# Kernel optimization log

Measured on AMD Instinct MI355X. Metric: run time of the kernel, lower is better.

Reference implementation:

```python
import jax, jax.numpy as jnp
import numpy as np
from math import factorial as fact

L, P, T, CIN, COUT, N = 4, 5, 15, 32, 32, 1000


def _cg(j1, m1, j2, m2, J, M):
    # Clebsch-Gordan coefficient <j1 m1 j2 m2 | J M> (integer args, Racah formula)
    if m1 + m2 != M or not (abs(j1 - j2) <= J <= j1 + j2):
        return 0.0
    if abs(m1) > j1 or abs(m2) > j2 or abs(M) > J:
        return 0.0
    pre = (2.0 * J + 1.0) * fact(J + j1 - j2) * fact(J - j1 + j2) * fact(j1 + j2 - J) / fact(j1 + j2 + J + 1)
    pre *= fact(J + M) * fact(J - M) * fact(j1 - m1) * fact(j1 + m1) * fact(j2 - m2) * fact(j2 + m2)
    s = 0.0
    for k in range(0, j1 + j2 - J + 1):
        d = (k, j1 + j2 - J - k, j1 - m1 - k, j2 + m2 - k, J - j2 + m1 + k, J - j1 - m2 + k)
        if min(d) < 0:
            continue
        den = 1.0
        for x in d:
            den *= fact(x)
        s += (-1.0) ** k / den
    return float(np.sqrt(pre) * s)


def _precompute(Ldeg):
    # Mirrors PrecomputingTensorsForConv6D
    tensors, coefs = [], []
    for l in range(Ldeg):
        for l1 in range(Ldeg):
            for l2 in range(abs(l - l1), min(Ldeg, l + l1 + 1)):
                coefs.append(8.0 * np.pi ** 2 / (2 * l1 + 1)
                             * np.sqrt((2 * l + 1) * (2 * l1 + 1) / (4.0 * np.pi * (2 * l2 + 1)))
                             * _cg(l, 0, l1, 0, l2, 0))
                T1 = np.zeros((l + 1, l1 + 1, l2 + 1)); T2 = np.zeros_like(T1); T3 = np.zeros_like(T1)
                for k in range(l + 1):
                    for k1 in range(l1 + 1):
                        if abs(k + k1) < l2 + 1:
                            T1[k, k1, k + k1] = _cg(l, k, l1, k1, l2, k + k1) * (-1) ** k1
                        if k1 > 0 and abs(k - k1) < l2 + 1:
                            if k - k1 >= 0:
                                T2[k, k1, k - k1] = _cg(l, k, l1, -k1, l2, k - k1) * (-1) ** l1
                            else:
                                T3[k, k1, k1 - k] = (-1) ** (k1 - k) * (-1) ** (l1 + l2) * _cg(l, k, l1, -k1, l2, k - k1)
                tensors.append((jnp.asarray(T1, jnp.float32), jnp.asarray(T2, jnp.float32), jnp.asarray(T3, jnp.float32)))
    return tensors, np.asarray(coefs, np.float64)

_TENSORS, _COEFS = _precompute(L)


def setup_inputs() -> dict:
    key = jax.random.key(0)
    ks = iter(jax.random.split(key, 64))
    inp = {}
    for l in range(L):
        inp[f"in{l}_real"] = 0.1 * jax.random.normal(next(ks), (N, T, l + 1, P, CIN), jnp.float32)
        inp[f"in{l}_imag"] = 0.1 * jax.random.normal(next(ks), (N, T, l + 1, P, CIN), jnp.float32)
    for l in range(L):
        inp[f"w{l}_real"] = 0.05 * jax.random.normal(next(ks), (l + 1, T, P, CIN, COUT), jnp.float32)
        inp[f"w{l}_imag"] = 0.05 * jax.random.normal(next(ks), (l + 1, T, P, CIN, COUT), jnp.float32)
    for l in range(L):
        inp[f"b{l}_real"] = jax.random.uniform(next(ks), (1, l + 1, P, COUT), jnp.float32, -0.05, 0.05)
        inp[f"b{l}_imag"] = jax.random.uniform(next(ks), (1, l + 1, P, COUT), jnp.float32, -0.05, 0.05)
    return inp


def _forward(ins, ws_raw, bs_raw):
    # Mask imaginary parts: weight order-0 row (k=0) and bias degree-0 component are zeroed,
    # exactly as the temp_term masks in build().
    ws, bs = [], []
    for l in range(L):
        wmask = jnp.ones((l + 1, 1, 1, 1, 1), jnp.float32).at[0].set(0.0)
        ws += [ws_raw[2 * l], ws_raw[2 * l + 1] * wmask]
        bmask = jnp.ones((1, l + 1, 1, 1), jnp.float32).at[:, 0].set(0.0)
        bs += [bs_raw[2 * l], bs_raw[2 * l + 1] * bmask]
    outputs = []
    itr = 0
    for l in range(L):
        out_r = 0.0
        out_i = 0.0
        for l1 in range(L):
            for l2 in range(abs(l - l1), min(L, l + l1 + 1)):
                c = float(_COEFS[itr])
                T1, T2, T3 = _TENSORS[itr]
                xr, xi = ins[2 * l2], ins[2 * l2 + 1]      # [N, T, l2+1, P, Cin]
                wr, wi = ws[2 * l1], ws[2 * l1 + 1]        # [l1+1, T, P, Cin, Cout]
                # complex CG contraction -> [N, l+1, P, Cout]
                out_r = out_r + c * jnp.einsum('lmk,ntkpi,mtpij->nlpj', T1 + T2 + T3, xr, wr)
                out_r = out_r - c * jnp.einsum('lmk,ntkpi,mtpij->nlpj', T1 - T2 + T3, xi, wi)
                out_i = out_i + c * jnp.einsum('lmk,ntkpi,mtpij->nlpj', T1 - T2 - T3, xr, wi)
                out_i = out_i + c * jnp.einsum('lmk,ntkpi,mtpij->nlpj', T1 + T2 - T3, xi, wr)
                itr += 1
        outputs.append(out_r + bs[2 * l])
        outputs.append(out_i + bs[2 * l + 1])
    return tuple(outputs)


def reference(in0_real, in0_imag, in1_real, in1_imag, in2_real, in2_imag, in3_real, in3_imag,
              w0_real, w0_imag, w1_real, w1_imag, w2_real, w2_imag, w3_real, w3_imag,
              b0_real, b0_imag, b1_real, b1_imag, b2_real, b2_imag, b3_real, b3_imag):
    ins = [in0_real, in0_imag, in1_real, in1_imag, in2_real, in2_imag, in3_real, in3_imag]
    ws = [w0_real, w0_imag, w1_real, w1_imag, w2_real, w2_imag, w3_real, w3_imag]
    bs = [b0_real, b0_imag, b1_real, b1_imag, b2_real, b2_imag, b3_real, b3_imag]
    return _forward(ins, ws, bs)
```

## Files before the change

### kernel.cpp

```cpp
#include <hip/hip_runtime.h>
#include <hip/hip_bf16.h>

#define NB   1000
#define NPAD 1024
#define TT   15
#define PP   5
#define CI   32
#define CO   32
#define KDIM 9600
#define MDIM 640
#define NCHUNK 300
#define NCOL   20
#define TABN  16384
#define KSTEPS 150
#define WTELEMS 1536000
#define XCVT_BLOCKS 24000
#define WTR_BLOCKS (WTELEMS / 256)
#define TAB_BLOCKS (TABN / 256)

typedef __attribute__((ext_vector_type(8))) short          bf16x8;
typedef __attribute__((ext_vector_type(8))) unsigned short ushort8;
typedef __attribute__((ext_vector_type(4))) float          f32x4;

struct Chunks {
  short ci[NCHUNK]; short l2[NCHUNK]; short t[NCHUNK]; short k2[NCHUNK];
  short xidx[NCHUNK]; short cls[NCHUNK]; int ns[NCHUNK]; int offc[NCHUNK];
};
constexpr Chunks mkchunks() {
  Chunks c{};
  int idx = 0;
  for (int l2 = 0; l2 < 4; ++l2)
    for (int ci = 0; ci < 2; ++ci)
      for (int t = 0; t < TT; ++t)
        for (int k2 = 0; k2 <= l2; ++k2) {
          c.ci[idx] = (short)ci; c.l2[idx] = (short)l2;
          c.t[idx] = (short)t;   c.k2[idx] = (short)k2;
          c.xidx[idx] = (short)(2 * l2 + ci);
          c.cls[idx]  = (short)(l2 * (l2 + 1) / 2 + k2);
          c.ns[idx]   = TT * (l2 + 1) * PP * CI;
          c.offc[idx] = (t * (l2 + 1) + k2) * PP * CI;
          ++idx;
        }
  return c;
}
__constant__ Chunks g_ck = mkchunks();

struct Cols { int l[NCOL]; int lm[NCOL]; int ci[NCOL]; long obase[NCOL]; };
constexpr Cols mkcols() {
  Cols c{};
  long acc = 0; int idx = 0;
  for (int l = 0; l < 4; ++l)
    for (int ci = 0; ci < 2; ++ci) {
      for (int lm = 0; lm <= l; ++lm) {
        c.l[idx] = l; c.lm[idx] = lm; c.ci[idx] = ci; c.obase[idx] = acc; ++idx;
      }
      acc += (long)NB * (l + 1) * PP * CO;
    }
  return c;
}
__constant__ Cols g_cols = mkcols();

constexpr int wtsize(int tensor) { return ((tensor >> 1) + 1) * TT * PP * CI * CO; }
struct WOffs { int off[8]; int sz[8]; };
constexpr WOffs mkwoffs() {
  WOffs w{}; int acc = 0;
  for (int i = 0; i < 8; ++i) { w.off[i] = acc; w.sz[i] = wtsize(i); acc += w.sz[i]; }
  return w;
}
__constant__ WOffs g_wo = mkwoffs();

__constant__ short g_l1of[10] = {0,1,1,2,2,2,3,3,3,3};
__constant__ short g_mof[10]  = {0,0,1,0,1,2,0,1,2,3};

__device__ double dfact(int n) { double r = 1.0; for (int i = 2; i <= n; ++i) r *= i; return r; }

__device__ double dcg(int j1, int m1, int j2, int m2, int J, int M) {
  if (m1 + m2 != M) return 0.0;
  int lo = j1 - j2; if (lo < 0) lo = -lo;
  if (J < lo || J > j1 + j2) return 0.0;
  int am1 = m1 < 0 ? -m1 : m1, am2 = m2 < 0 ? -m2 : m2, aM = M < 0 ? -M : M;
  if (am1 > j1 || am2 > j2 || aM > J) return 0.0;
  double pre = (2.0 * J + 1.0) * dfact(J + j1 - j2) * dfact(J - j1 + j2) * dfact(j1 + j2 - J)
               / dfact(j1 + j2 + J + 1);
  pre *= dfact(J + M) * dfact(J - M) * dfact(j1 - m1) * dfact(j1 + m1) * dfact(j2 - m2) * dfact(j2 + m2);
  double s = 0.0;
  for (int k = 0; k <= j1 + j2 - J; ++k) {
    int d1 = j1 + j2 - J - k, d2 = j1 - m1 - k, d3 = j2 + m2 - k,
        d4 = J - j2 + m1 + k, d5 = J - j1 - m2 + k;
    if (d1 < 0 || d2 < 0 || d3 < 0 || d4 < 0 || d5 < 0) continue;
    double den = dfact(k) * dfact(d1) * dfact(d2) * dfact(d3) * dfact(d4) * dfact(d5);
    s += ((k & 1) ? -1.0 : 1.0) / den;
  }
  return sqrt(pre) * s;
}

struct PArgs { const float* w[8]; const float* x[8]; float* wt; float* tab; unsigned short* xb; };

__global__ __launch_bounds__(256) void k_prep(PArgs A) {
  const int bx = blockIdx.x, tid = threadIdx.x;
  if (bx < XCVT_BLOCKS) {
    int slot = bx * 256 + tid;
    int i8 = slot % 1200;
    int rest = slot / 1200;
    int n = rest & (NPAD - 1);
    int p = rest >> 10;
    int kk = i8 * 8;
    ushort8 o;
    if (n < NB) {
      int chunk = kk >> 5;
      const float* xp = A.x[g_ck.xidx[chunk]] + (size_t)n * g_ck.ns[chunk]
                        + g_ck.offc[chunk] + p * CI + (kk & 31);
      float4 v0 = *(const float4*)xp;
      float4 v1 = *(const float4*)(xp + 4);
      float f[8] = {v0.x, v0.y, v0.z, v0.w, v1.x, v1.y, v1.z, v1.w};
      #pragma unroll
      for (int e = 0; e < 8; ++e) {
        unsigned u = __float_as_uint(f[e]);
        u += 0x7fff + ((u >> 16) & 1);
        o[e] = (unsigned short)(u >> 16);
      }
    } else {
      #pragma unroll
      for (int e = 0; e < 8; ++e) o[e] = 0;
    }
    *(ushort8*)(A.xb + ((size_t)(p * NPAD + n)) * KDIM + kk) = o;
  } else if (bx < XCVT_BLOCKS + WTR_BLOCKS) {
    int e = (bx - XCVT_BLOCKS) * 256 + tid;
    int tensor = 0;
    #pragma unroll
    for (int q = 1; q < 8; ++q) if (e >= g_wo.off[q]) tensor = q;
    int le = e - g_wo.off[tensor];
    int i = le & 31;
    int t = (le >> 5) % TT;
    int r = le / (32 * TT);
    int j = r & 31;
    int p = (r >> 5) % PP;
    int m = r / (32 * PP);
    A.wt[e] = A.w[tensor][(((m * TT + t) * PP + p) * CI + i) * CO + j];
  } else {
    int idx = (bx - XCVT_BLOCKS - WTR_BLOCKS) * 256 + tid;
    int k2 = idx & 3, m = (idx >> 2) & 3, lm = (idx >> 4) & 3, l2 = (idx >> 6) & 3,
        l1 = (idx >> 8) & 3, l = (idx >> 10) & 3, combo = (idx >> 12) & 3;
    float v = 0.f;
    int dlo = l - l1; if (dlo < 0) dlo = -dlo;
    bool valid = (lm <= l) && (m <= l1) && (k2 <= l2) && (l2 >= dlo) && (l2 <= l + l1);
    if (valid) {
      const double PI = 3.14159265358979323846;
      double coef = 8.0 * PI * PI / (2.0 * l1 + 1.0)
                    * sqrt((2.0 * l + 1.0) * (2.0 * l1 + 1.0) / (4.0 * PI * (2.0 * l2 + 1.0)))
                    * dcg(l, 0, l1, 0, l2, 0);
      double t1 = 0.0, t2 = 0.0, t3 = 0.0;
      if (k2 == lm + m)
        t1 = dcg(l, lm, l1, m, l2, k2) * ((m & 1) ? -1.0 : 1.0);
      if (m > 0 && lm - m >= 0 && k2 == lm - m)
        t2 = dcg(l, lm, l1, -m, l2, lm - m) * ((l1 & 1) ? -1.0 : 1.0);
      if (m > 0 && lm - m < 0 && k2 == m - lm)
        t3 = (((m - lm) & 1) ? -1.0 : 1.0) * (((l1 + l2) & 1) ? -1.0 : 1.0)
             * dcg(l, lm, l1, -m, l2, lm - m);
      double r = 0.0;
      if (combo == 0) r =  coef * (t1 + t2 + t3);
      else if (combo == 1) r = -coef * (t1 - t2 + t3);
      else if (combo == 2) r =  coef * (t1 - t2 - t3);
      else r = coef * (t1 + t2 - t3);
      v = (float)r;
    }
    A.tab[idx] = v;
  }
}

struct FArgs { const float* wt; const float* tab; unsigned short* weffT; };

__global__ __launch_bounds__(256) void k_fold(FArgs A) {
  const int tid = threadIdx.x;
  const int mo = blockIdx.x, p = blockIdx.y;
  const int j = mo & 31, col = mo >> 5;
  const int l = g_cols.l[col], lm = g_cols.lm[col], cio = g_cols.ci[col];
  __shared__ float ldsW[2][10][480];
  __shared__ float ldsC[2][10][10];

  for (int e = tid; e < 2 * 10 * 480; e += 256) {
    int ti = e % 480;
    int rowid = e / 480;
    int wci = rowid / 10, r = rowid % 10;
    int l1 = g_l1of[r], m = g_mof[r];
    ldsW[wci][r][ti] = A.wt[g_wo.off[2 * l1 + wci] + m * (PP * CO * TT * CI)
                            + (p * CO + j) * (TT * CI) + ti];
  }
  if (tid < 200) {
    int r = tid % 10, clk = (tid / 10) % 10, ci = tid / 100;
    int l1 = g_l1of[r], m = g_mof[r];
    int l2 = g_l1of[clk], k2 = g_mof[clk];
    int combo = cio * 2 + ci, wci = cio ^ ci;
    float v = 0.f;
    int dlo = l - l1; if (dlo < 0) dlo = -dlo;
    if (l2 >= dlo && l2 <= l + l1 && m <= l1 && k2 <= l2)
      v = A.tab[(((((combo * 4 + l) * 4 + l1) * 4 + l2) * 4 + lm) * 4 + m) * 4 + k2];
    if (wci == 1 && m == 0) v = 0.f;
    ldsC[ci][clk][r] = v;
  }
  __syncthreads();

  unsigned short* dst = A.weffT + ((size_t)(p * MDIM + mo)) * KDIM;
  for (int kk = tid; kk < KDIM; kk += 256) {
    int chunk = kk >> 5, i = kk & 31;
    int ci = g_ck.ci[chunk], t = g_ck.t[chunk], cls = g_ck.cls[chunk];
    int wci = cio ^ ci;
    float s = 0.f;
    #pragma unroll
    for (int r = 0; r < 10; ++r)
      s += ldsC[ci][cls][r] * ldsW[wci][r][t * 32 + i];
    unsigned u = __float_as_uint(s);
    u += 0x7fff + ((u >> 16) & 1);
    dst[kk] = (unsigned short)(u >> 16);
  }
}

__device__ __forceinline__ void gl_lds16(const void* g, void* l) {
  __builtin_amdgcn_global_load_lds(
      (const __attribute__((address_space(1))) unsigned int*)g,
      (__attribute__((address_space(3))) unsigned int*)l, 16, 0, 0);
}

struct GArgs { const unsigned short* xb; const unsigned short* weffT; float* partial; int nsplit; };

__global__ __launch_bounds__(256, 4) void k_gemm(GArgs A) {
  const int tid = threadIdx.x;
  const int lane = tid & 63;
  const int wv = tid >> 6, wr = wv >> 1, wc = wv & 1;
  const int n0 = blockIdx.x * 128, mo0 = blockIdx.y * 128;
  const int zz = blockIdx.z;
  const int NS = A.nsplit;
  const int p = zz / NS, sp = zz % NS;
  const int bsteps = KSTEPS / NS, rem = KSTEPS % NS;
  const int mysteps = bsteps + (sp < rem ? 1 : 0);
  const int sstart = sp * bsteps + (sp < rem ? sp : rem);

  __shared__ __align__(16) unsigned short sA[128 * 64];
  __shared__ __align__(16) unsigned short sB[128 * 64];
  f32x4 acc[4][4] = {};

  int aoff[4];
  #pragma unroll
  for (int u = 0; u < 4; ++u) {
    int s = u * 256 + tid;
    int row = s >> 3;
    int qs = (s & 7) ^ (row & 7);
    aoff[u] = row * KDIM + qs * 8;
  }
  const unsigned short* xbase = A.xb + (size_t)p * NPAD * KDIM + (size_t)n0 * KDIM + sstart * 64;
  const unsigned short* wbase = A.weffT + (size_t)p * MDIM * KDIM + (size_t)mo0 * KDIM + sstart * 64;

  for (int cc = 0; cc < mysteps; ++cc) {
    const unsigned short* xs = xbase + cc * 64;
    const unsigned short* ws = wbase + cc * 64;
    #pragma unroll
    for (int u = 0; u < 4; ++u) {
      gl_lds16(xs + aoff[u], (void*)(sA + (u * 256 + tid) * 8));
      gl_lds16(ws + aoff[u], (void*)(sB + (u * 256 + tid) * 8));
    }
    __syncthreads();
    #pragma unroll
    for (int ks = 0; ks < 2; ++ks) {
      const int q = ks * 4 + (lane >> 4);
      bf16x8 af[4], bfr[4];
      #pragma unroll
      for (int m = 0; m < 4; ++m) {
        int ra = wr * 64 + m * 16 + (lane & 15);
        af[m] = *(const bf16x8*)(sA + ra * 64 + ((q ^ (ra & 7)) << 3));
      }
      #pragma unroll
      for (int n = 0; n < 4; ++n) {
        int rb = wc * 64 + n * 16 + (lane & 15);
        bfr[n] = *(const bf16x8*)(sB + rb * 64 + ((q ^ (rb & 7)) << 3));
      }
      #pragma unroll
      for (int m = 0; m < 4; ++m)
        #pragma unroll
        for (int n = 0; n < 4; ++n)
          acc[m][n] = __builtin_amdgcn_mfma_f32_16x16x32_bf16(af[m], bfr[n], acc[m][n], 0, 0, 0);
    }
    __syncthreads();
  }

  float* pout = A.partial + (size_t)zz * (NPAD * MDIM);
  #pragma unroll
  for (int m = 0; m < 4; ++m) {
    #pragma unroll
    for (int nn = 0; nn < 4; ++nn) {
      int mo = mo0 + wc * 64 + nn * 16 + (lane & 15);
      #pragma unroll
      for (int r = 0; r < 4; ++r) {
        int n = n0 + wr * 64 + m * 16 + (lane >> 4) * 4 + r;
        pout[(size_t)n * MDIM + mo] = acc[m][nn][r];
      }
    }
  }
}

struct RArgs { const float* partial; const float* b[8]; float* out; int nsplit; };

__global__ __launch_bounds__(256) void k_red(RArgs A) {
  int e4 = blockIdx.x * 256 + threadIdx.x;
  if (e4 >= NB * (MDIM / 4) * PP) return;
  int mo4 = e4 % (MDIM / 4);
  int rest = e4 / (MDIM / 4);
  int n = rest % NB;
  int p = rest / NB;
  int mo = mo4 * 4;
  float4 s = make_float4(0.f, 0.f, 0.f, 0.f);
  for (int sp = 0; sp < A.nsplit; ++sp) {
    float4 v = *(const float4*)&A.partial[((size_t)(p * A.nsplit + sp) * NPAD + n) * MDIM + mo];
    s.x += v.x; s.y += v.y; s.z += v.z; s.w += v.w;
  }
  int colid = mo >> 5, j = mo & 31;
  int l = g_cols.l[colid], lmv = g_cols.lm[colid], cio = g_cols.ci[colid];
  long base = g_cols.obase[colid];
  float4 bias = *(const float4*)&A.b[2 * l + cio][(lmv * PP + p) * CO + j];
  if (cio == 1 && lmv == 0) bias = make_float4(0.f, 0.f, 0.f, 0.f);
  float4 o = make_float4(s.x + bias.x, s.y + bias.y, s.z + bias.z, s.w + bias.w);
  *(float4*)&A.out[base + (((size_t)n * (l + 1) + lmv) * PP + p) * CO + j] = o;
}

extern "C" void kernel_launch(void* const* d_in, const int* in_sizes, int n_in,
                              void* d_out, int out_size, void* d_ws, size_t ws_size,
                              hipStream_t stream) {
  float* tab = (float*)d_ws;
  float* wt  = tab + TABN;
  unsigned short* weffT = (unsigned short*)(wt + WTELEMS);
  unsigned short* xb    = weffT + (size_t)PP * MDIM * KDIM;
  float* partial = (float*)(xb + (size_t)PP * NPAD * KDIM);

  size_t base_bytes = (size_t)TABN * 4 + (size_t)WTELEMS * 4
                    + (size_t)PP * MDIM * KDIM * 2 + (size_t)PP * NPAD * KDIM * 2;
  size_t per_split = (size_t)PP * NPAD * MDIM * 4;
  int NS = 1;
  for (int c = 5; c >= 2; --c)
    if (ws_size >= base_bytes + (size_t)c * per_split) { NS = c; break; }

  PArgs pa;
  for (int i = 0; i < 8; ++i) pa.w[i] = (const float*)d_in[8 + i];
  for (int i = 0; i < 8; ++i) pa.x[i] = (const float*)d_in[i];
  pa.wt = wt; pa.tab = tab; pa.xb = xb;
  k_prep<<<dim3(XCVT_BLOCKS + WTR_BLOCKS + TAB_BLOCKS), dim3(256), 0, stream>>>(pa);

  FArgs fa;
  fa.wt = wt; fa.tab = (const float*)tab; fa.weffT = weffT;
  k_fold<<<dim3(MDIM, PP), dim3(256), 0, stream>>>(fa);

  GArgs ga;
  ga.xb = xb; ga.weffT = weffT; ga.partial = partial; ga.nsplit = NS;
  k_gemm<<<dim3(8, 5, 5 * NS), dim3(256), 0, stream>>>(ga);

  RArgs ra;
  ra.partial = partial; ra.out = (float*)d_out; ra.nsplit = NS;
  for (int i = 0; i < 8; ++i) ra.b[i] = (const float*)d_in[16 + i];
  k_red<<<dim3((NB * (MDIM / 4) * PP + 255) / 256), dim3(256), 0, stream>>>(ra);
}
```

Measured before the change: 267.1 us.

## Widen x conversion per thread, LDS-tile weight transpose, remap GEMM blocks per XCD

The x-to-bf16 conversion now has each thread handle a full 32-channel chunk with eight float4 loads and four 16-byte stores, which cuts the block count. The weight transpose now goes through a shared-memory tile, so both global reads and writes are coalesced instead of scattered gathers. The GEMM launch is flattened to 1D and block indices are remapped so consecutive blocks on the same XCD (blockIdx mod 8) share the same z-slice, which should improve L2 reuse. The catch is added index arithmetic and a shared-memory allocation in k_prep that every branch of the kernel pays for, not just the transpose branch.

```diff
diff --git a/kernel.cpp b/kernel.cpp
--- a/kernel.cpp
+++ b/kernel.cpp
@@ -14,8 +14,8 @@
 #define TABN  16384
 #define KSTEPS 150
 #define WTELEMS 1536000
-#define XCVT_BLOCKS 24000
-#define WTR_BLOCKS (WTELEMS / 256)
+#define XCVT_BLOCKS 6000
+#define WTRX_BLOCKS 300
 #define TAB_BLOCKS (TABN / 256)
 
 typedef __attribute__((ext_vector_type(8))) short          bf16x8;
@@ -71,6 +71,8 @@
 
 __constant__ short g_l1of[10] = {0,1,1,2,2,2,3,3,3,3};
 __constant__ short g_mof[10]  = {0,0,1,0,1,2,0,1,2,3};
+__constant__ short g_wtT[20] = {0,1,2,2,3,3,4,4,4,5,5,5,6,6,6,6,7,7,7,7};
+__constant__ short g_wtM[20] = {0,0,0,1,0,1,0,1,2,0,1,2,0,1,2,3,0,1,2,3};
 
 __device__ double dfact(int n) { double r = 1.0; for (int i = 2; i <= n; ++i) r *= i; return r; }
 
@@ -98,47 +100,65 @@
 
 __global__ __launch_bounds__(256) void k_prep(PArgs A) {
   const int bx = blockIdx.x, tid = threadIdx.x;
+  __shared__ float lds[5][32][33];
+
   if (bx < XCVT_BLOCKS) {
-    int slot = bx * 256 + tid;
-    int i8 = slot % 1200;
-    int rest = slot / 1200;
+    int g = bx * 256 + tid;
+    int chunk = g % 300;
+    int rest = g / 300;
     int n = rest & (NPAD - 1);
     int p = rest >> 10;
-    int kk = i8 * 8;
-    ushort8 o;
+    ushort8* dst = (ushort8*)(A.xb + ((size_t)(p * NPAD + n)) * KDIM + chunk * 32);
     if (n < NB) {
-      int chunk = kk >> 5;
       const float* xp = A.x[g_ck.xidx[chunk]] + (size_t)n * g_ck.ns[chunk]
-                        + g_ck.offc[chunk] + p * CI + (kk & 31);
-      float4 v0 = *(const float4*)xp;
-      float4 v1 = *(const float4*)(xp + 4);
-      float f[8] = {v0.x, v0.y, v0.z, v0.w, v1.x, v1.y, v1.z, v1.w};
-      #pragma unroll
-      for (int e = 0; e < 8; ++e) {
-        unsigned u = __float_as_uint(f[e]);
-        u += 0x7fff + ((u >> 16) & 1);
-        o[e] = (unsigned short)(u >> 16);
+                        + g_ck.offc[chunk] + p * CI;
+      float4 v[8];
+      #pragma unroll
+      for (int e = 0; e < 8; ++e) v[e] = *(const float4*)(xp + 4 * e);
+      #pragma unroll
+      for (int q = 0; q < 4; ++q) {
+        float4 a = v[2 * q], b = v[2 * q + 1];
+        float fa[8] = {a.x, a.y, a.z, a.w, b.x, b.y, b.z, b.w};
+        ushort8 o;
+        #pragma unroll
+        for (int e = 0; e < 8; ++e) {
+          unsigned u = __float_as_uint(fa[e]);
+          u += 0x7fff + ((u >> 16) & 1);
+          o[e] = (unsigned short)(u >> 16);
+        }
+        dst[q] = o;
       }
     } else {
-      #pragma unroll
-      for (int e = 0; e < 8; ++e) o[e] = 0;
-    }
-    *(ushort8*)(A.xb + ((size_t)(p * NPAD + n)) * KDIM + kk) = o;
-  } else if (bx < XCVT_BLOCKS + WTR_BLOCKS) {
-    int e = (bx - XCVT_BLOCKS) * 256 + tid;
-    int tensor = 0;
-    #pragma unroll
-    for (int q = 1; q < 8; ++q) if (e >= g_wo.off[q]) tensor = q;
-    int le = e - g_wo.off[tensor];
-    int i = le & 31;
-    int t = (le >> 5) % TT;
-    int r = le / (32 * TT);
-    int j = r & 31;
-    int p = (r >> 5) % PP;
-    int m = r / (32 * PP);
-    A.wt[e] = A.w[tensor][(((m * TT + t) * PP + p) * CI + i) * CO + j];
+      ushort8 z = {0,0,0,0,0,0,0,0};
+      #pragma unroll
+      for (int q = 0; q < 4; ++q) dst[q] = z;
+    }
+  } else if (bx < XCVT_BLOCKS + WTRX_BLOCKS) {
+    int b = bx - XCVT_BLOCKS;
+    int t_ = b % TT;
+    int mrow = b / TT;
+    int tensor = g_wtT[mrow], m = g_wtM[mrow];
+    const float* src = A.w[tensor] + (size_t)(m * TT + t_) * (PP * CI * CO);
+    #pragma unroll
+    for (int k = 0; k < 5; ++k) {
+      int f = tid + k * 256;
+      float4 v = *(const float4*)(src + f * 4);
+      int elem = f * 4;
+      int p = elem >> 10, rem = elem & 1023;
+      int i = rem >> 5, j0 = rem & 31;
+      lds[p][i][j0] = v.x; lds[p][i][j0 + 1] = v.y;
+      lds[p][i][j0 + 2] = v.z; lds[p][i][j0 + 3] = v.w;
+    }
+    __syncthreads();
+    float* dst = A.wt + g_wo.off[tensor] + (size_t)m * (PP * CO * TT * CI) + t_ * CI;
+    #pragma unroll
+    for (int k = 0; k < 20; ++k) {
+      int e = tid + k * 256;
+      int i = e & 31, pj = e >> 5;
+      dst[pj * (TT * CI) + i] = lds[pj >> 5][i][pj & 31];
+    }
   } else {
-    int idx = (bx - XCVT_BLOCKS - WTR_BLOCKS) * 256 + tid;
+    int idx = (bx - XCVT_BLOCKS - WTRX_BLOCKS) * 256 + tid;
     int k2 = idx & 3, m = (idx >> 2) & 3, lm = (idx >> 4) & 3, l2 = (idx >> 6) & 3,
         l1 = (idx >> 8) & 3, l = (idx >> 10) & 3, combo = (idx >> 12) & 3;
     float v = 0.f;
@@ -227,9 +247,20 @@
   const int tid = threadIdx.x;
   const int lane = tid & 63;
   const int wv = tid >> 6, wr = wv >> 1, wc = wv & 1;
-  const int n0 = blockIdx.x * 128, mo0 = blockIdx.y * 128;
-  const int zz = blockIdx.z;
   const int NS = A.nsplit;
+
+  const int x = blockIdx.x & 7;
+  const int jj = blockIdx.x >> 3;
+  const int perx = 25 * NS;
+  const int full = perx / 40;
+  int zz, slot;
+  if (jj < full * 40) { zz = x + 8 * (jj / 40); slot = jj % 40; }
+  else {
+    int leftover = perx - full * 40;
+    int idx = x * leftover + (jj - full * 40);
+    zz = full * 8 + idx / 40; slot = idx % 40;
+  }
+  const int n0 = (slot & 7) * 128, mo0 = (slot >> 3) * 128;
   const int p = zz / NS, sp = zz % NS;
   const int bsteps = KSTEPS / NS, rem = KSTEPS % NS;
   const int mysteps = bsteps + (sp < rem ? 1 : 0);
@@ -341,7 +372,7 @@
   for (int i = 0; i < 8; ++i) pa.w[i] = (const float*)d_in[8 + i];
   for (int i = 0; i < 8; ++i) pa.x[i] = (const float*)d_in[i];
   pa.wt = wt; pa.tab = tab; pa.xb = xb;
-  k_prep<<<dim3(XCVT_BLOCKS + WTR_BLOCKS + TAB_BLOCKS), dim3(256), 0, stream>>>(pa);
+  k_prep<<<dim3(XCVT_BLOCKS + WTRX_BLOCKS + TAB_BLOCKS), dim3(256), 0, stream>>>(pa);
 
   FArgs fa;
   fa.wt = wt; fa.tab = (const float*)tab; fa.weffT = weffT;
@@ -349,7 +380,7 @@
 
   GArgs ga;
   ga.xb = xb; ga.weffT = weffT; ga.partial = partial; ga.nsplit = NS;
-  k_gemm<<<dim3(8, 5, 5 * NS), dim3(256), 0, stream>>>(ga);
+  k_gemm<<<dim3(200 * NS), dim3(256), 0, stream>>>(ga);
 
   RArgs ra;
   ra.partial = partial; ra.out = (float*)d_out; ra.nsplit = NS;
```

Result: faster. 236.4 us (-11.5%).
